# Kernel optimization log

Measured on AMD Instinct MI355X. Metric: run time of the kernel, lower is better.

Reference implementation:

```python
import jax, jax.numpy as jnp
import numpy as np

STRIDES = [8, 16, 32, 64, 128]
HW = [(100, 128), (50, 64), (25, 32), (13, 16), (7, 8)]
SCORE_THR = 0.05
IOU_THR = 0.6
MAX_DET = 1000
MAX_OUT = 100  # fixed pad size in _post_process


def _coords(h, w, stride):
    # FCOS coords_fmap2orig: center of each cell in original image coords
    sx = jnp.arange(w, dtype=jnp.float32) * stride + stride // 2
    sy = jnp.arange(h, dtype=jnp.float32) * stride + stride // 2
    yy, xx = jnp.meshgrid(sy, sx, indexing='ij')
    return jnp.stack([xx.reshape(-1), yy.reshape(-1)], axis=-1)  # [h*w, 2]


def _reshape_cat(feats):
    # list of [B,C,h,w] -> [B, sum(h*w), C]
    outs = [f.transpose(0, 2, 3, 1).reshape(f.shape[0], -1, f.shape[1]) for f in feats]
    return jnp.concatenate(outs, axis=1)


def _nms_single(scores, classes, boxes):
    # scores [N] (sorted desc), classes [N] int, boxes [N,4]; greedy DIoU-NMS
    N = scores.shape[0]
    valid = scores >= SCORE_THR
    # batched_nms: offset boxes by class so cross-class boxes never overlap
    max_coord = jnp.max(jnp.where(valid[:, None], boxes, -jnp.inf))
    offs = classes.astype(boxes.dtype) * (max_coord + 1.0)
    b = boxes + offs[:, None]
    x1, y1, x2, y2 = b[:, 0], b[:, 1], b[:, 2], b[:, 3]
    areas = (x2 - x1 + 1.0) * (y2 - y1 + 1.0)
    cx, cy = (x1 + x2) * 0.5, (y1 + y2) * 0.5
    xmin = jnp.maximum(x1[:, None], x1[None, :]); ymin = jnp.maximum(y1[:, None], y1[None, :])
    xmax = jnp.minimum(x2[:, None], x2[None, :]); ymax = jnp.minimum(y2[:, None], y2[None, :])
    inter = jnp.clip(xmax - xmin, 0) * jnp.clip(ymax - ymin, 0)
    iou = inter / (areas[:, None] + areas[None, :] - inter)
    inter_diag = (cx[:, None] - cx[None, :]) ** 2 + (cy[:, None] - cy[None, :]) ** 2
    oxmin = jnp.minimum(x1[:, None], x1[None, :]); oymin = jnp.minimum(y1[:, None], y1[None, :])
    oxmax = jnp.maximum(x2[:, None], x2[None, :]); oymax = jnp.maximum(y2[:, None], y2[None, :])
    outer_diag = (oxmax - oxmin) ** 2 + (oymax - oymin) ** 2
    diou = iou - inter_diag / jnp.maximum(outer_diag, 1e-12)
    idxs = jnp.arange(N)

    def body(i, keep):
        sup = keep[i] & (idxs > i) & (diou[i] > IOU_THR)
        return keep & (~sup)

    keep = jax.lax.fori_loop(0, N, body, valid)
    # kept boxes in descending-score order, padded with -2 to MAX_OUT
    rank = jnp.cumsum(keep) - 1
    pos = jnp.where(keep, jnp.minimum(rank, MAX_OUT), MAX_OUT)  # slot MAX_OUT is dumped
    out_s = jnp.full((MAX_OUT + 1,), -2.0, scores.dtype).at[pos].set(jnp.where(keep, scores, -2.0))[:MAX_OUT]
    out_c = jnp.full((MAX_OUT + 1,), -2, classes.dtype).at[pos].set(jnp.where(keep, classes, -2))[:MAX_OUT]
    out_b = jnp.full((MAX_OUT + 1, 4), -2.0, boxes.dtype).at[pos].set(jnp.where(keep[:, None], boxes, -2.0))[:MAX_OUT]
    return out_s, out_c, out_b


def _forward(cls_feats, reg_feats):
    cls_logits = _reshape_cat(cls_feats)          # [B, L, C]
    reg_preds = _reshape_cat(reg_feats)           # [B, L, 4]
    coords = jnp.concatenate([_coords(h, w, s) for (h, w), s in zip(HW, STRIDES)], axis=0)
    cls_preds = jax.nn.sigmoid(cls_logits)
    cls_scores = jnp.max(cls_preds, axis=-1)      # [B, L]
    cls_classes = jnp.argmax(cls_preds, axis=-1) + 1
    x1y1 = coords[None] - reg_preds[..., :2]
    x2y2 = coords[None] + reg_preds[..., 2:]
    boxes = jnp.concatenate([x1y1, x2y2], axis=-1)  # [B, L, 4]
    max_num = min(MAX_DET, cls_scores.shape[-1])
    topv, topi = jax.lax.top_k(cls_scores, max_num)  # sorted descending
    top_c = jnp.take_along_axis(cls_classes, topi, axis=1)
    top_b = jnp.take_along_axis(boxes, topi[..., None], axis=1)
    return jax.vmap(_nms_single)(topv, top_c, top_b)


def setup_inputs() -> dict:
    key = jax.random.key(0)
    ks = jax.random.split(key, 16)
    inp = {}
    C = 80
    for i, (h, w) in enumerate(HW):
        inp[f'cls{i}'] = jax.random.normal(ks[i], (16, C, h, w), dtype=jnp.float32)
        # ltrb offsets scaled so boxes are realistically sized and overlap
        inp[f'reg{i}'] = jax.random.uniform(ks[5 + i], (16, 4, h, w), dtype=jnp.float32) * 64.0
    inp['boxes_anchor'] = jax.random.normal(ks[10], (16, 100, 4), dtype=jnp.float32)
    inp['labels_anchor'] = jax.random.randint(ks[11], (16, 100), 0, 80)
    inp['score_anchor'] = jax.random.uniform(ks[12], (16, 100), dtype=jnp.float32)
    return inp


def reference(cls0, cls1, cls2, cls3, cls4, reg0, reg1, reg2, reg3, reg4,
              boxes_anchor, labels_anchor, score_anchor):
    # nms_anchor (boxes_anchor, labels_anchor, score_anchor) is consumed but
    # does not affect the output in the original forward.
    scores, classes, boxes = _forward([cls0, cls1, cls2, cls3, cls4],
                                      [reg0, reg1, reg2, reg3, reg4])
    return scores, classes, boxes
```

## Files before the change

kernel.cpp:

```cpp
#include <hip/hip_runtime.h>
#include <math.h>

typedef unsigned int u32;
typedef unsigned long long u64;

#define BB 16
#define NANCH 17064
#define NGRP 4266
#define NTOP 1000
#define NWORD 16
#define NOUT 100
#define NBIN 65536
#define NSPLIT 17

__device__ __forceinline__ u32 fmap(float v) {
    u32 u = __float_as_uint(v);
    return (u & 0x80000000u) ? ~u : (u | 0x80000000u);
}
__device__ __forceinline__ float funmap(u32 u) {
    u32 b = (u & 0x80000000u) ? (u & 0x7FFFFFFFu) : ~u;
    return __uint_as_float(b);
}

__global__ void __launch_bounds__(256) k_anchor(
        const float* __restrict__ c0, const float* __restrict__ c1,
        const float* __restrict__ c2, const float* __restrict__ c3,
        const float* __restrict__ c4,
        const float* __restrict__ r0, const float* __restrict__ r1,
        const float* __restrict__ r2, const float* __restrict__ r3,
        const float* __restrict__ r4,
        u32* __restrict__ akey, int* __restrict__ aclass,
        float* __restrict__ abox, u32* __restrict__ ghist) {
    int tid = threadIdx.x;
    int b = blockIdx.y;
    int gt = blockIdx.x * 256 + tid;
    if (gt >= 4 * NGRP) return;
    int p = gt >> 2, cs = gt & 3;
    int a = p * 4;

    const float *cp, *rp;
    int loc, wl, h, stride, half;
    if (a < 12800)      { loc = a;         wl = 7; h = 100; stride = 8;   half = 4;  cp = c0; rp = r0; }
    else if (a < 16000) { loc = a - 12800; wl = 6; h = 50;  stride = 16;  half = 8;  cp = c1; rp = r1; }
    else if (a < 16800) { loc = a - 16000; wl = 5; h = 25;  stride = 32;  half = 16; cp = c2; rp = r2; }
    else if (a < 17008) { loc = a - 16800; wl = 4; h = 13;  stride = 64;  half = 32; cp = c3; rp = r3; }
    else                { loc = a - 17008; wl = 3; h = 7;   stride = 128; half = 64; cp = c4; rp = r4; }
    int y = loc >> wl, x = loc & ((1 << wl) - 1);
    int hw = h << wl, hwq = hw >> 2;

    const float4* cb4 = (const float4*)(cp + (size_t)b * 80 * hw +
                                        (size_t)cs * 20 * hw + loc);
    int cbase = cs * 20;
    float4 v = cb4[0];
    float m0 = v.x, m1 = v.y, m2 = v.z, m3 = v.w;
    int a0 = cbase, a1 = cbase, a2 = cbase, a3 = cbase;
#pragma unroll
    for (int c = 1; c < 20; ++c) {
        float4 u = cb4[(size_t)c * hwq];
        int cc = cbase + c;
        if (u.x > m0) { m0 = u.x; a0 = cc; }
        if (u.y > m1) { m1 = u.y; a1 = cc; }
        if (u.z > m2) { m2 = u.z; a2 = cc; }
        if (u.w > m3) { m3 = u.w; a3 = cc; }
    }
    {
        bool low = (cs & 1) == 0;
        float pm; int pa; bool tk;
        pm = __shfl_xor(m0, 1); pa = __shfl_xor(a0, 1);
        tk = low ? (m0 >= pm) : (m0 > pm); m0 = tk ? m0 : pm; a0 = tk ? a0 : pa;
        pm = __shfl_xor(m1, 1); pa = __shfl_xor(a1, 1);
        tk = low ? (m1 >= pm) : (m1 > pm); m1 = tk ? m1 : pm; a1 = tk ? a1 : pa;
        pm = __shfl_xor(m2, 1); pa = __shfl_xor(a2, 1);
        tk = low ? (m2 >= pm) : (m2 > pm); m2 = tk ? m2 : pm; a2 = tk ? a2 : pa;
        pm = __shfl_xor(m3, 1); pa = __shfl_xor(a3, 1);
        tk = low ? (m3 >= pm) : (m3 > pm); m3 = tk ? m3 : pm; a3 = tk ? a3 : pa;
    }
    {
        bool low = (cs & 2) == 0;
        float pm; int pa; bool tk;
        pm = __shfl_xor(m0, 2); pa = __shfl_xor(a0, 2);
        tk = low ? (m0 >= pm) : (m0 > pm); m0 = tk ? m0 : pm; a0 = tk ? a0 : pa;
        pm = __shfl_xor(m1, 2); pa = __shfl_xor(a1, 2);
        tk = low ? (m1 >= pm) : (m1 > pm); m1 = tk ? m1 : pm; a1 = tk ? a1 : pa;
        pm = __shfl_xor(m2, 2); pa = __shfl_xor(a2, 2);
        tk = low ? (m2 >= pm) : (m2 > pm); m2 = tk ? m2 : pm; a2 = tk ? a2 : pa;
        pm = __shfl_xor(m3, 2); pa = __shfl_xor(a3, 2);
        tk = low ? (m3 >= pm) : (m3 > pm); m3 = tk ? m3 : pm; a3 = tk ? a3 : pa;
    }
    if (cs == 0) {
        const float4* rb4 = (const float4*)(rp + (size_t)b * 4 * hw + loc);
        float4 gl = rb4[0], gt_ = rb4[hwq], gr = rb4[2 * hwq], gb = rb4[3 * hwq];

        int idx = b * NANCH + a;
        u32 km0 = fmap(m0), km1 = fmap(m1), km2 = fmap(m2), km3 = fmap(m3);
        *(uint4*)(akey + idx) = make_uint4(km0, km1, km2, km3);
        *(int4*)(aclass + idx) = make_int4(a0 + 1, a1 + 1, a2 + 1, a3 + 1);
        u32* gh = ghist + (size_t)b * NBIN;
        atomicAdd(&gh[km0 >> 16], 1u);
        atomicAdd(&gh[km1 >> 16], 1u);
        atomicAdd(&gh[km2 >> 16], 1u);
        atomicAdd(&gh[km3 >> 16], 1u);
        float cy = (float)(y * stride + half);
        float cx0 = (float)(x * stride + half);
        float gls[4] = {gl.x, gl.y, gl.z, gl.w};
        float gts[4] = {gt_.x, gt_.y, gt_.z, gt_.w};
        float grs[4] = {gr.x, gr.y, gr.z, gr.w};
        float gbs[4] = {gb.x, gb.y, gb.z, gb.w};
#pragma unroll
        for (int k = 0; k < 4; ++k) {
            float cx = cx0 + (float)(k * stride);
            *(float4*)(abox + (size_t)(idx + k) * 4) =
                make_float4(cx - gls[k], cy - gts[k], cx + grs[k], cy + gbs[k]);
        }
    }
}

__global__ void __launch_bounds__(256) k_thresh(const u32* __restrict__ ghist,
                                                u32* __restrict__ thr) {
    __shared__ u32 seg[256];
    __shared__ u32 binv[256];
    __shared__ int Gmax, Tmax;
    int b = blockIdx.x, t = threadIdx.x;
    const u32* gh = ghist + (size_t)b * NBIN;
    u32 s = 0;
    const uint4* g4 = (const uint4*)(gh + t * 256);
#pragma unroll 8
    for (int j = 0; j < 64; ++j) {
        uint4 q = g4[j];
        s += q.x + q.y + q.z + q.w;
    }
    seg[t] = s;
    if (t == 0) { Gmax = 0; }
    __syncthreads();
    for (int off = 1; off < 256; off <<= 1) {
        u32 v = seg[t];
        u32 add = (t + off < 256) ? seg[t + off] : 0u;
        __syncthreads();
        seg[t] = v + add;
        __syncthreads();
    }
    if (seg[t] >= NTOP) atomicMax(&Gmax, t);
    __syncthreads();
    int G = Gmax;
    u32 hi = (G < 255) ? seg[G + 1] : 0u;
    binv[t] = gh[G * 256 + t];
    if (t == 0) { Tmax = G * 256; }
    __syncthreads();
    for (int off = 1; off < 256; off <<= 1) {
        u32 v = binv[t];
        u32 add = (t + off < 256) ? binv[t + off] : 0u;
        __syncthreads();
        binv[t] = v + add;
        __syncthreads();
    }
    if (binv[t] + hi >= NTOP) atomicMax(&Tmax, G * 256 + t);
    __syncthreads();
    if (t == 0) thr[b] = (u32)Tmax;
}

__global__ void __launch_bounds__(256) k_compact(const u32* __restrict__ akey,
                                                 const u32* __restrict__ thr,
                                                 u32* __restrict__ ccnt,
                                                 u64* __restrict__ cand) {
    __shared__ u32 lcnt, baseoff;
    int b = blockIdx.y, s = blockIdx.x, t = threadIdx.x;
    if (t == 0) lcnt = 0;
    __syncthreads();
    u32 T = thr[b];

    int base = s * 1024;
    int n = min(1024, NANCH - base);
    u32 kk[4]; u32 pos[4]; bool m[4] = {false, false, false, false};
    if (4 * t < n) {
        uint4 k4 = *(const uint4*)(akey + (size_t)b * NANCH + base + 4 * t);
        kk[0] = k4.x; kk[1] = k4.y; kk[2] = k4.z; kk[3] = k4.w;
#pragma unroll
        for (int i = 0; i < 4; ++i) {
            m[i] = (kk[i] >> 16) >= T;
            if (m[i]) pos[i] = atomicAdd(&lcnt, 1u);
        }
    }
    __syncthreads();
    if (t == 0) baseoff = atomicAdd(&ccnt[b], lcnt);
    __syncthreads();
    u32 bo = baseoff;
    u64* cb = cand + (size_t)b * NANCH;
#pragma unroll
    for (int i = 0; i < 4; ++i) {
        if (m[i])
            cb[bo + pos[i]] =
                ((u64)kk[i] << 32) | (u64)(0xFFFFFFFFu - (u32)(base + 4 * t + i));
    }
}

__global__ void __launch_bounds__(256) k_rank(
        const u64* __restrict__ cand, const u32* __restrict__ ccnt,
        const int* __restrict__ aclass, const float* __restrict__ abox,
        float* __restrict__ tscore, int* __restrict__ tclass,
        float* __restrict__ tbox, u32* __restrict__ maxcU) {
    __shared__ u64 tile[2048];
    int b = blockIdx.y, tid = threadIdx.x;
    int C = (int)ccnt[b];
    const u64* ck = cand + (size_t)b * NANCH;
    for (int base = blockIdx.x * 256; base < C; base += gridDim.x * 256) {
        int i = base + tid;
        bool have = i < C;
        u64 my = have ? ck[i] : 0ull;
        int rank = 0;
        for (int t0 = 0; t0 < C; t0 += 2048) {
            int nt = min(2048, C - t0);
            __syncthreads();
            for (int j = tid; j < nt; j += 256) tile[j] = ck[t0 + j];
            __syncthreads();
            int r0 = 0, r1 = 0, r2 = 0, r3 = 0, r4 = 0, r5 = 0, r6 = 0, r7 = 0;
            int j = 0;
            for (; j + 8 <= nt; j += 8) {
                u64 v0 = tile[j + 0], v1 = tile[j + 1];
                u64 v2 = tile[j + 2], v3 = tile[j + 3];
                u64 v4 = tile[j + 4], v5 = tile[j + 5];
                u64 v6 = tile[j + 6], v7 = tile[j + 7];
                r0 += v0 > my; r1 += v1 > my; r2 += v2 > my; r3 += v3 > my;
                r4 += v4 > my; r5 += v5 > my; r6 += v6 > my; r7 += v7 > my;
            }
            for (; j < nt; ++j) r0 += tile[j] > my;
            rank += ((r0 + r1) + (r2 + r3)) + ((r4 + r5) + (r6 + r7));
        }
        u32 mymax = 0;
        if (have && rank < NTOP) {
            u32 a = 0xFFFFFFFFu - (u32)(my & 0xFFFFFFFFull);
            int src = b * NANCH + (int)a;
            int dst = b * NTOP + rank;
            float logit = funmap((u32)(my >> 32));
            float sc = 1.0f / (1.0f + expf(-logit));
            float b0 = abox[src * 4 + 0], b1 = abox[src * 4 + 1];
            float b2 = abox[src * 4 + 2], b3 = abox[src * 4 + 3];
            tscore[dst] = sc;
            tclass[dst] = aclass[src];
            tbox[dst * 4 + 0] = b0;
            tbox[dst * 4 + 1] = b1;
            tbox[dst * 4 + 2] = b2;
            tbox[dst * 4 + 3] = b3;
            if (sc >= 0.05f)
                mymax = fmap(fmaxf(fmaxf(b0, b1), fmaxf(b2, b3)));
        }
        for (int off = 32; off > 0; off >>= 1) {
            u32 o = (u32)__shfl_down((int)mymax, off);
            mymax = mymax > o ? mymax : o;
        }
        if ((tid & 63) == 0) atomicMax(&maxcU[b], mymax);
    }
}

__global__ void k_sup(const float* __restrict__ tbox, const int* __restrict__ tclass,
                      const u32* __restrict__ maxcU, u64* __restrict__ sup) {
    int u = blockIdx.x, b = blockIdx.y;
    int ti = 0, rem = u;
    while (rem >= NWORD - ti) { rem -= NWORD - ti; ++ti; }
    int tj = ti + rem;
    int t = threadIdx.x;
    __shared__ double jx1[64], jy1[64], jx2[64], jy2[64], jcx[64], jcy[64], jar[64];
    double mc1 = (double)funmap(maxcU[b]) + 1.0;
    int j = tj * 64 + t;
    if (j < NTOP) {
        const float* bx = tbox + (size_t)(b * NTOP + j) * 4;
        double o = (double)tclass[b * NTOP + j] * mc1;
        double x1 = (double)bx[0] + o, y1 = (double)bx[1] + o;
        double x2 = (double)bx[2] + o, y2 = (double)bx[3] + o;
        jx1[t] = x1; jy1[t] = y1; jx2[t] = x2; jy2[t] = y2;
        jcx[t] = (x1 + x2) * 0.5; jcy[t] = (y1 + y2) * 0.5;
        jar[t] = (x2 - x1 + 1.0) * (y2 - y1 + 1.0);
    }
    __syncthreads();
    int i = ti * 64 + t;
    if (i >= NTOP) return;
    const float* bx = tbox + (size_t)(b * NTOP + i) * 4;
    double o = (double)tclass[b * NTOP + i] * mc1;
    double ix1 = (double)bx[0] + o, iy1 = (double)bx[1] + o;
    double ix2 = (double)bx[2] + o, iy2 = (double)bx[3] + o;
    double icx = (ix1 + ix2) * 0.5, icy = (iy1 + iy2) * 0.5;
    double iar = (ix2 - ix1 + 1.0) * (iy2 - iy1 + 1.0);
    u64 bits = 0;
    int jbase = tj * 64;
    for (int jj = 0; jj < 64; ++jj) {
        int jg = jbase + jj;
        if (jg >= NTOP) break;
        if (jg <= i) continue;
        double xm = fmax(ix1, jx1[jj]), ym = fmax(iy1, jy1[jj]);
        double xM = fmin(ix2, jx2[jj]), yM = fmin(iy2, jy2[jj]);
        double inter = fmax(xM - xm, 0.0) * fmax(yM - ym, 0.0);
        double U = iar + jar[jj] - inter;
        double dx = icx - jcx[jj], dy = icy - jcy[jj];
        double idg = dx * dx + dy * dy;
        double ox = fmax(ix2, jx2[jj]) - fmin(ix1, jx1[jj]);
        double oy = fmax(iy2, jy2[jj]) - fmin(iy1, jy1[jj]);
        double odg = fmax(ox * ox + oy * oy, 1e-12);
        if (inter * odg - idg * U > 0.6 * (U * odg)) bits |= (1ull << jj);
    }
    sup[(size_t)(b * NTOP + i) * NWORD + tj] = bits;
}

__global__ void __launch_bounds__(64) k_scan(
        const u64* __restrict__ sup, const float* __restrict__ tscore,
        const int* __restrict__ tclass, const float* __restrict__ tbox,
        float* __restrict__ out) {
    int b = blockIdx.x, lane = threadIdx.x;
    __shared__ u64 lds[64 * 17];
    __shared__ int kept_lds[NOUT];
    const u64* supb = sup + (size_t)b * NTOP * NWORD;
    u64 remw = 0;
    int kept = 0;
    for (int t = 0; t < NWORD; ++t) {
        int r0 = t * 64;
#pragma unroll
        for (int q = 0; q < 16; ++q) {
            int e = q * 64 + lane;
            int rr = r0 + (e >> 4), w = e & 15;
            u64 v = (rr < NTOP) ? supb[(size_t)rr * 16 + w] : 0ull;
            lds[(e >> 4) * 17 + w] = v;
        }
        __syncthreads();
        int r = r0 + lane;
        float s = (r < NTOP) ? tscore[b * NTOP + r] : -1.0f;
        u64 vmask = __ballot(s >= 0.05f);
        u64 M = lds[lane * 17 + t];
        u64 rem_t = __shfl(remw, t);
        u64 cnd = vmask & ~rem_t;
        u64 keepmask = 0;
        while (cnd) {
            int k = __ffsll(cnd) - 1;
            keepmask |= 1ull << k;
            if (lane == 0) kept_lds[kept] = r0 + k;
            ++kept;
            if (kept >= NOUT) break;
            u64 Mk = __shfl(M, k);
            cnd &= ~(Mk | (1ull << k));
        }
        if (lane < NWORD) {
            u64 km = keepmask;
            while (km) {
                int k = __ffsll(km) - 1;
                km &= km - 1;
                remw |= lds[k * 17 + lane];
            }
        }
        __syncthreads();
        if (kept >= NOUT) break;
    }
    float* os = out + b * NOUT;
    float* oc = out + BB * NOUT + b * NOUT;
    float* ob = out + 2 * BB * NOUT + (size_t)b * NOUT * 4;
    for (int i = lane; i < NOUT; i += 64) { os[i] = -2.0f; oc[i] = -2.0f; }
    for (int i = lane; i < NOUT * 4; i += 64) ob[i] = -2.0f;
    __syncthreads();
    int ncopy = kept < NOUT ? kept : NOUT;
    for (int r = lane; r < ncopy; r += 64) {
        int i = kept_lds[r];
        os[r] = tscore[b * NTOP + i];
        oc[r] = (float)tclass[b * NTOP + i];
        ob[r * 4 + 0] = tbox[(size_t)(b * NTOP + i) * 4 + 0];
        ob[r * 4 + 1] = tbox[(size_t)(b * NTOP + i) * 4 + 1];
        ob[r * 4 + 2] = tbox[(size_t)(b * NTOP + i) * 4 + 2];
        ob[r * 4 + 3] = tbox[(size_t)(b * NTOP + i) * 4 + 3];
    }
}

extern "C" void kernel_launch(void* const* d_in, const int* in_sizes, int n_in,
                              void* d_out, int out_size, void* d_ws, size_t ws_size,
                              hipStream_t stream) {
    (void)in_sizes; (void)n_in; (void)out_size; (void)ws_size;
    const float* cls[5];
    const float* reg[5];
    for (int i = 0; i < 5; ++i) {
        cls[i] = (const float*)d_in[2 * i];
        reg[i] = (const float*)d_in[2 * i + 1];
    }
    float* out = (float*)d_out;

    char* ws = (char*)d_ws;
    u32* ghist = (u32*)ws;           ws += (size_t)BB * NBIN * sizeof(u32);
    u32* ccnt = (u32*)ws;            ws += 64;
    u32* maxcU = (u32*)ws;           ws += 64;
    size_t zbytes = (size_t)BB * NBIN * sizeof(u32) + 128;
    u32* thr = (u32*)ws;             ws += 64;
    u64* cand = (u64*)ws;            ws += (size_t)BB * NANCH * sizeof(u64);
    u64* sup = (u64*)ws;             ws += (size_t)BB * NTOP * NWORD * sizeof(u64);
    u32* akey = (u32*)ws;            ws += (size_t)BB * NANCH * sizeof(u32);
    int* aclass = (int*)ws;          ws += (size_t)BB * NANCH * sizeof(int);
    float* abox = (float*)ws;        ws += (size_t)BB * NANCH * 4 * sizeof(float);
    float* tscore = (float*)ws;      ws += (size_t)BB * NTOP * sizeof(float);
    int* tclass = (int*)ws;          ws += (size_t)BB * NTOP * sizeof(int);
    float* tbox = (float*)ws;        ws += (size_t)BB * NTOP * 4 * sizeof(float);

    hipMemsetAsync(ghist, 0, zbytes, stream);

    k_anchor<<<dim3((4 * NGRP + 255) / 256, BB), 256, 0, stream>>>(
        cls[0], cls[1], cls[2], cls[3], cls[4],
        reg[0], reg[1], reg[2], reg[3], reg[4],
        akey, aclass, abox, ghist);
    k_thresh<<<BB, 256, 0, stream>>>(ghist, thr);
    k_compact<<<dim3(NSPLIT, BB), 256, 0, stream>>>(akey, thr, ccnt, cand);
    k_rank<<<dim3(8, BB), 256, 0, stream>>>(cand, ccnt, aclass, abox,
                                            tscore, tclass, tbox, maxcU);
    k_sup<<<dim3(136, BB), 64, 0, stream>>>(tbox, tclass, maxcU, sup);
    k_scan<<<BB, 64, 0, stream>>>(sup, tscore, tclass, tbox, out);
}
```

Baseline: 268.9 us.

## Replace global atomic histogram with two-pass shared-memory radix select for top-k threshold

```diff
diff --git a/kernel.cpp b/kernel.cpp
--- a/kernel.cpp
+++ b/kernel.cpp
@@ -10,7 +10,7 @@
 #define NTOP 1000
 #define NWORD 16
 #define NOUT 100
-#define NBIN 65536
+#define NBIN13 8192
 #define NSPLIT 17
 
 __device__ __forceinline__ u32 fmap(float v) {
@@ -30,7 +30,7 @@
         const float* __restrict__ r2, const float* __restrict__ r3,
         const float* __restrict__ r4,
         u32* __restrict__ akey, int* __restrict__ aclass,
-        float* __restrict__ abox, u32* __restrict__ ghist) {
+        float* __restrict__ abox) {
     int tid = threadIdx.x;
     int b = blockIdx.y;
     int gt = blockIdx.x * 256 + tid;
@@ -50,13 +50,22 @@
 
     const float4* cb4 = (const float4*)(cp + (size_t)b * 80 * hw +
                                         (size_t)cs * 20 * hw + loc);
+    float4 buf[20];
+#pragma unroll
+    for (int c = 0; c < 20; ++c) buf[c] = cb4[(size_t)c * hwq];
+    const float4* rb4 = (const float4*)(rp + (size_t)b * 4 * hw + loc);
+    float4 gl, gt_, gr, gb;
+    if (cs == 0) {
+        gl = rb4[0]; gt_ = rb4[hwq]; gr = rb4[2 * hwq]; gb = rb4[3 * hwq];
+    }
+    __builtin_amdgcn_sched_barrier(0);
+
     int cbase = cs * 20;
-    float4 v = cb4[0];
-    float m0 = v.x, m1 = v.y, m2 = v.z, m3 = v.w;
+    float m0 = buf[0].x, m1 = buf[0].y, m2 = buf[0].z, m3 = buf[0].w;
     int a0 = cbase, a1 = cbase, a2 = cbase, a3 = cbase;
 #pragma unroll
     for (int c = 1; c < 20; ++c) {
-        float4 u = cb4[(size_t)c * hwq];
+        float4 u = buf[c];
         int cc = cbase + c;
         if (u.x > m0) { m0 = u.x; a0 = cc; }
         if (u.y > m1) { m1 = u.y; a1 = cc; }
@@ -88,18 +97,9 @@
         tk = low ? (m3 >= pm) : (m3 > pm); m3 = tk ? m3 : pm; a3 = tk ? a3 : pa;
     }
     if (cs == 0) {
-        const float4* rb4 = (const float4*)(rp + (size_t)b * 4 * hw + loc);
-        float4 gl = rb4[0], gt_ = rb4[hwq], gr = rb4[2 * hwq], gb = rb4[3 * hwq];
-
         int idx = b * NANCH + a;
-        u32 km0 = fmap(m0), km1 = fmap(m1), km2 = fmap(m2), km3 = fmap(m3);
-        *(uint4*)(akey + idx) = make_uint4(km0, km1, km2, km3);
+        *(uint4*)(akey + idx) = make_uint4(fmap(m0), fmap(m1), fmap(m2), fmap(m3));
         *(int4*)(aclass + idx) = make_int4(a0 + 1, a1 + 1, a2 + 1, a3 + 1);
-        u32* gh = ghist + (size_t)b * NBIN;
-        atomicAdd(&gh[km0 >> 16], 1u);
-        atomicAdd(&gh[km1 >> 16], 1u);
-        atomicAdd(&gh[km2 >> 16], 1u);
-        atomicAdd(&gh[km3 >> 16], 1u);
         float cy = (float)(y * stride + half);
         float cx0 = (float)(x * stride + half);
         float gls[4] = {gl.x, gl.y, gl.z, gl.w};
@@ -115,22 +115,33 @@
     }
 }
 
-__global__ void __launch_bounds__(256) k_thresh(const u32* __restrict__ ghist,
-                                                u32* __restrict__ thr) {
+__global__ void __launch_bounds__(256) k_refine(const u32* __restrict__ akey,
+                                                u32* __restrict__ thr,
+                                                u32* __restrict__ ccnt,
+                                                u32* __restrict__ maxcU) {
+    __shared__ u32 h1[NBIN13];
     __shared__ u32 seg[256];
-    __shared__ u32 binv[256];
-    __shared__ int Gmax, Tmax;
+    __shared__ u32 binb[32];
+    __shared__ int Gs;
+    __shared__ u32 T13s, As;
     int b = blockIdx.x, t = threadIdx.x;
-    const u32* gh = ghist + (size_t)b * NBIN;
+    const uint4* ak4 = (const uint4*)(akey + (size_t)b * NANCH);
+
+    for (int i = t; i < NBIN13; i += 256) h1[i] = 0;
+    if (t == 0) Gs = 0;
+    __syncthreads();
+    for (int i = t; i < NANCH / 4; i += 256) {
+        uint4 k4 = ak4[i];
+        atomicAdd(&h1[k4.x >> 19], 1u);
+        atomicAdd(&h1[k4.y >> 19], 1u);
+        atomicAdd(&h1[k4.z >> 19], 1u);
+        atomicAdd(&h1[k4.w >> 19], 1u);
+    }
+    __syncthreads();
     u32 s = 0;
-    const uint4* g4 = (const uint4*)(gh + t * 256);
-#pragma unroll 8
-    for (int j = 0; j < 64; ++j) {
-        uint4 q = g4[j];
-        s += q.x + q.y + q.z + q.w;
-    }
+#pragma unroll
+    for (int j = 0; j < 32; ++j) s += h1[t * 32 + ((j + t) & 31)];
     seg[t] = s;
-    if (t == 0) { Gmax = 0; }
     __syncthreads();
     for (int off = 1; off < 256; off <<= 1) {
         u32 v = seg[t];
@@ -139,23 +150,63 @@
         seg[t] = v + add;
         __syncthreads();
     }
-    if (seg[t] >= NTOP) atomicMax(&Gmax, t);
-    __syncthreads();
-    int G = Gmax;
+    if (seg[t] >= NTOP) atomicMax(&Gs, t);
+    __syncthreads();
+    int G = Gs;
     u32 hi = (G < 255) ? seg[G + 1] : 0u;
-    binv[t] = gh[G * 256 + t];
-    if (t == 0) { Tmax = G * 256; }
+    if (t < 32) binb[t] = h1[G * 32 + t];
+    __syncthreads();
+    if (t == 0) {
+        u32 acc = hi, A = hi;
+        int T13 = G * 32;
+        for (int i = 31; i >= 0; --i) {
+            A = acc;
+            acc += binb[i];
+            if (acc >= NTOP) { T13 = G * 32 + i; break; }
+        }
+        T13s = (u32)T13; As = A;
+        Gs = 0;
+    }
+    __syncthreads();
+    u32 T13 = T13s, A = As;
+    for (int i = t; i < NBIN13; i += 256) h1[i] = 0;
+    __syncthreads();
+    for (int i = t; i < NANCH / 4; i += 256) {
+        uint4 k4 = ak4[i];
+        if ((k4.x >> 19) == T13) atomicAdd(&h1[(k4.x >> 6) & (NBIN13 - 1)], 1u);
+        if ((k4.y >> 19) == T13) atomicAdd(&h1[(k4.y >> 6) & (NBIN13 - 1)], 1u);
+        if ((k4.z >> 19) == T13) atomicAdd(&h1[(k4.z >> 6) & (NBIN13 - 1)], 1u);
+        if ((k4.w >> 19) == T13) atomicAdd(&h1[(k4.w >> 6) & (NBIN13 - 1)], 1u);
+    }
+    __syncthreads();
+    u32 target = NTOP - A;
+    u32 s2 = 0;
+#pragma unroll
+    for (int j = 0; j < 32; ++j) s2 += h1[t * 32 + ((j + t) & 31)];
+    seg[t] = s2;
     __syncthreads();
     for (int off = 1; off < 256; off <<= 1) {
-        u32 v = binv[t];
-        u32 add = (t + off < 256) ? binv[t + off] : 0u;
-        __syncthreads();
-        binv[t] = v + add;
-        __syncthreads();
-    }
-    if (binv[t] + hi >= NTOP) atomicMax(&Tmax, G * 256 + t);
-    __syncthreads();
-    if (t == 0) thr[b] = (u32)Tmax;
+        u32 v = seg[t];
+        u32 add = (t + off < 256) ? seg[t + off] : 0u;
+        __syncthreads();
+        seg[t] = v + add;
+        __syncthreads();
+    }
+    if (seg[t] >= target) atomicMax(&Gs, t);
+    __syncthreads();
+    int G2 = Gs;
+    u32 hi2 = (G2 < 255) ? seg[G2 + 1] : 0u;
+    if (t == 0) {
+        u32 acc = hi2;
+        int t2 = G2 * 32;
+        for (int i = 31; i >= 0; --i) {
+            acc += h1[G2 * 32 + i];
+            if (acc >= target) { t2 = G2 * 32 + i; break; }
+        }
+        thr[b] = (T13 << 13) | (u32)t2;
+        ccnt[b] = 0;
+        maxcU[b] = 0;
+    }
 }
 
 __global__ void __launch_bounds__(256) k_compact(const u32* __restrict__ akey,
@@ -176,7 +227,7 @@
         kk[0] = k4.x; kk[1] = k4.y; kk[2] = k4.z; kk[3] = k4.w;
 #pragma unroll
         for (int i = 0; i < 4; ++i) {
-            m[i] = (kk[i] >> 16) >= T;
+            m[i] = (kk[i] >> 6) >= T;
             if (m[i]) pos[i] = atomicAdd(&lcnt, 1u);
         }
     }
@@ -377,11 +428,9 @@
     float* out = (float*)d_out;
 
     char* ws = (char*)d_ws;
-    u32* ghist = (u32*)ws;           ws += (size_t)BB * NBIN * sizeof(u32);
+    u32* thr = (u32*)ws;             ws += 64;
     u32* ccnt = (u32*)ws;            ws += 64;
     u32* maxcU = (u32*)ws;           ws += 64;
-    size_t zbytes = (size_t)BB * NBIN * sizeof(u32) + 128;
-    u32* thr = (u32*)ws;             ws += 64;
     u64* cand = (u64*)ws;            ws += (size_t)BB * NANCH * sizeof(u64);
     u64* sup = (u64*)ws;             ws += (size_t)BB * NTOP * NWORD * sizeof(u64);
     u32* akey = (u32*)ws;            ws += (size_t)BB * NANCH * sizeof(u32);
@@ -391,15 +440,13 @@
     int* tclass = (int*)ws;          ws += (size_t)BB * NTOP * sizeof(int);
     float* tbox = (float*)ws;        ws += (size_t)BB * NTOP * 4 * sizeof(float);
 
-    hipMemsetAsync(ghist, 0, zbytes, stream);
-
     k_anchor<<<dim3((4 * NGRP + 255) / 256, BB), 256, 0, stream>>>(
         cls[0], cls[1], cls[2], cls[3], cls[4],
         reg[0], reg[1], reg[2], reg[3], reg[4],
-        akey, aclass, abox, ghist);
-    k_thresh<<<BB, 256, 0, stream>>>(ghist, thr);
+        akey, aclass, abox);
+    k_refine<<<BB, 256, 0, stream>>>(akey, thr, ccnt, maxcU);
     k_compact<<<dim3(NSPLIT, BB), 256, 0, stream>>>(akey, thr, ccnt, cand);
-    k_rank<<<dim3(8, BB), 256, 0, stream>>>(cand, ccnt, aclass, abox,
+    k_rank<<<dim3(5, BB), 256, 0, stream>>>(cand, ccnt, aclass, abox,
                                             tscore, tclass, tbox, maxcU);
     k_sup<<<dim3(136, BB), 64, 0, stream>>>(tbox, tclass, maxcU, sup);
     k_scan<<<BB, 64, 0, stream>>>(sup, tscore, tclass, tbox, out);
```

New measurement: 230.9 us. -14.1%, faster.
